# Kernel tuning notes

Hardware: AMD Instinct MI355X
Metric: run time of the kernel (lower is better)

Reference implementation:

```python
import jax, jax.numpy as jnp
import numpy as np

B, N, C, H = 4, 1024, 768, 12
HD = C // H
EPS = 1e-5


def setup_inputs() -> dict:
    key = jax.random.key(0)
    ks = jax.random.split(key, 6)
    before = jax.random.normal(ks[0], (B, N, C), dtype=jnp.float32)
    after = jax.random.normal(ks[1], (B, N, C), dtype=jnp.float32)
    W_qkv = jax.random.normal(ks[2], (3 * C, C), dtype=jnp.float32) * (1.0 / np.sqrt(C))
    ln_g = jnp.ones((HD,), dtype=jnp.float32)
    ln_b = jnp.zeros((HD,), dtype=jnp.float32)
    W_proj = jax.random.normal(ks[3], (C, C), dtype=jnp.float32) * (1.0 / np.sqrt(C))
    b_proj = jnp.zeros((C,), dtype=jnp.float32)
    return {"before": before, "after": after, "W_qkv": W_qkv, "ln_g": ln_g,
            "ln_b": ln_b, "W_proj": W_proj, "b_proj": b_proj}


def _qkv_norm(x, W_qkv, ln_g, ln_b):
    # x: [B,N,C] -> qkv: [3,B,H,N,hd] with LayerNorm over head_dim
    qkv = (x @ W_qkv.T).reshape(B, N, 3, H, HD).transpose(2, 0, 3, 1, 4)
    mu = jnp.mean(qkv, axis=-1, keepdims=True)
    var = jnp.var(qkv, axis=-1, keepdims=True)
    qkv = (qkv - mu) * jax.lax.rsqrt(var + EPS) * ln_g + ln_b
    return qkv[0], qkv[1], qkv[2]


def _cross_attn(q, k, v, scale, W_proj, b_proj):
    # q,k,v: [B,H,N,hd]
    attn = jax.nn.softmax(jnp.einsum('bhqd,bhkd->bhqk', q, k) * scale, axis=-1)
    ctx = jnp.einsum('bhqk,bhkd->bhqd', attn, v)  # [B,H,N,hd]
    ctx = ctx.transpose(0, 2, 1, 3).reshape(B, N, C)
    ctx = ctx @ W_proj.T + b_proj
    # NOTE: original adds q.reshape(B,N,C) WITHOUT transposing heads back; replicate faithfully.
    return ctx + q.reshape(B, N, C)


def reference(before, after, W_qkv, ln_g, ln_b, W_proj, b_proj):
    scale = HD ** (-0.5)
    q_b, k_b, v_b = _qkv_norm(before, W_qkv, ln_g, ln_b)
    q_a, k_a, v_a = _qkv_norm(after, W_qkv, ln_g, ln_b)
    context_a = _cross_attn(q_b, k_a, v_a, scale, W_proj, b_proj)
    context_b = _cross_attn(q_a, k_b, v_b, scale, W_proj, b_proj)
    return (context_b, context_a)
```

## Files before the change

### kernel.cpp

```cpp
#include <hip/hip_runtime.h>


typedef __bf16 bf16x8 __attribute__((ext_vector_type(8)));
typedef float  f32x4  __attribute__((ext_vector_type(4)));
typedef unsigned int u32x4 __attribute__((ext_vector_type(4)));
typedef unsigned short us;

#define MFMA16(a, b, c) __builtin_amdgcn_mfma_f32_16x16x32_bf16(a, b, c, 0, 0, 0)

#define C1F 0.18033688011112042f
#define INV_C1F 5.545177444479562f

__device__ __forceinline__ us f2bf(float f) {
  unsigned int u = __builtin_bit_cast(unsigned int, f);
  u += 0x7FFFu + ((u >> 16) & 1u);
  return (us)(u >> 16);
}
__device__ __forceinline__ float bf2f(us h) {
  unsigned int u = ((unsigned int)h) << 16;
  return __builtin_bit_cast(float, u);
}
__device__ __forceinline__ bf16x8 ld16(const us* p) {
  return __builtin_bit_cast(bf16x8, *(const u32x4*)p);
}
__device__ __forceinline__ unsigned int pkbf(float lo, float hi) {
  return __builtin_amdgcn_perm(__builtin_bit_cast(unsigned int, hi),
                               __builtin_bit_cast(unsigned int, lo),
                               0x07060302u);
}

#define CH 136

__global__ __launch_bounds__(256) void k_convert(
    const float* __restrict__ before, const float* __restrict__ after,
    const float* __restrict__ wqkv, const float* __restrict__ wproj,
    us* __restrict__ ws) {
  int t = blockIdx.x * 256 + threadIdx.x;
  us* dst; int u;
  if (t < 786432)       { u = t;           dst = ws; }
  else if (t < 1007616) { u = t - 786432;  dst = ws + 6291456; }
  else                  { u = t - 1007616; dst = ws + 8060928; }
  int l15 = u & 15, c2 = u >> 4;
  int kc = c2 % 96, mt = c2 / 96;
  int row = mt * 16 + l15;
  const float* srow;
  if (t < 786432)       srow = row < 4096 ? before + (size_t)row * 768
                                          : after + (size_t)(row - 4096) * 768;
  else if (t < 1007616) srow = wqkv + (size_t)row * 768;
  else                  srow = wproj + (size_t)row * 768;
  const float4* s4 = (const float4*)(srow + kc * 8);
  float4 a = s4[0], b = s4[1];
  union { u32x4 v; us s[8]; } o;
  o.s[0] = f2bf(a.x); o.s[1] = f2bf(a.y); o.s[2] = f2bf(a.z); o.s[3] = f2bf(a.w);
  o.s[4] = f2bf(b.x); o.s[5] = f2bf(b.y); o.s[6] = f2bf(b.z); o.s[7] = f2bf(b.w);
  *(u32x4*)(dst + (size_t)c2 * 128 + l15 * 8) = o.v;
}

template <int MT>
__device__ __forceinline__ void gemm_mainloop(
    const us* __restrict__ A, const us* __restrict__ B,
    int m0, int n0, us* As, us* Bs, f32x4 (&acc)[MT / 32][4]) {
  constexpr int AJ = MT / 32;
  constexpr int NITER = 12;
  const int tid = threadIdx.x, lane = tid & 63, w = tid >> 6;
  const int quad = lane >> 4, l15 = lane & 15;
  const int wm = (w >> 1) * (MT / 2), wn = (w & 1) * 64;
  u32x4 ra[2][AJ], rb[2][4];

  auto load_regs = [&](int s, int k0) {
#pragma unroll
    for (int j = 0; j < AJ; ++j) {
      int u = w * AJ + j;
      ra[s][j] = *(const u32x4*)(A + ((size_t)((m0 >> 4) + (u >> 1)) * 96
                                      + (k0 >> 3) + (u & 1) * 4) * 128 + lane * 8);
    }
#pragma unroll
    for (int j = 0; j < 4; ++j) {
      int u = w * 4 + j;
      rb[s][j] = *(const u32x4*)(B + ((size_t)((n0 >> 4) + (u >> 1)) * 96
                                      + (k0 >> 3) + (u & 1) * 4) * 128 + lane * 8);
    }
  };
  auto store_regs = [&](int s) {
#pragma unroll
    for (int j = 0; j < AJ; ++j) {
      int slot = (w * AJ + j) * 4 + quad;
      *(u32x4*)(As + slot * CH + l15 * 8) = ra[s][j];
    }
#pragma unroll
    for (int j = 0; j < 4; ++j) {
      int slot = (w * 4 + j) * 4 + quad;
      *(u32x4*)(Bs + slot * CH + l15 * 8) = rb[s][j];
    }
  };

  load_regs(0, 0);
  load_regs(1, 64);
  store_regs(0);
  __syncthreads();

#pragma unroll
  for (int it = 0; it < NITER; ++it) {
    if (it + 2 < NITER) load_regs(it & 1, (it + 2) * 64);
#pragma unroll
    for (int ks = 0; ks < 2; ++ks) {
      bf16x8 af[AJ], bfr[4];
#pragma unroll
      for (int mf = 0; mf < AJ; ++mf)
        af[mf] = ld16(As + (((wm >> 4) + mf) * 8 + ks * 4 + quad) * CH + l15 * 8);
#pragma unroll
      for (int nf = 0; nf < 4; ++nf)
        bfr[nf] = ld16(Bs + (((wn >> 4) + nf) * 8 + ks * 4 + quad) * CH + l15 * 8);
#pragma unroll
      for (int mf = 0; mf < AJ; ++mf)
#pragma unroll
        for (int nf = 0; nf < 4; ++nf)
          acc[mf][nf] = MFMA16(af[mf], bfr[nf], acc[mf][nf]);
    }
    __syncthreads();
    if (it + 1 < NITER) {
      store_regs((it + 1) & 1);
      __syncthreads();
    }
  }
}

__global__ __launch_bounds__(256) void k_gemm_qkv(
    const us* __restrict__ A, const us* __restrict__ B, us* __restrict__ Cqk,
    us* __restrict__ Vg, const float* __restrict__ g, const float* __restrict__ bb) {
  __shared__ us As[64 * CH];
  __shared__ us Bs[64 * CH];
  const int lane = threadIdx.x & 63, w = threadIdx.x >> 6;
  const int quad = lane >> 4, l15 = lane & 15;
  const int m0 = blockIdx.x * 128, n0 = blockIdx.y * 128;
  const int wm = (w >> 1) * 64, wn = (w & 1) * 64;
  f32x4 acc[4][4] = {};
  gemm_mainloop<128>(A, B, m0, n0, As, Bs, acc);

  float gl[4], bl[4];
#pragma unroll
  for (int nf = 0; nf < 4; ++nf) { gl[nf] = g[nf * 16 + l15]; bl[nf] = bb[nf * 16 + l15]; }

  if ((n0 + wn) < 1536) {
    const float qs = (n0 + wn) < 768 ? C1F : 1.0f;
#pragma unroll
    for (int mf = 0; mf < 4; ++mf)
#pragma unroll
      for (int r = 0; r < 4; ++r) {
        float s1 = acc[mf][0][r] + acc[mf][1][r] + acc[mf][2][r] + acc[mf][3][r];
        float s2 = acc[mf][0][r] * acc[mf][0][r] + acc[mf][1][r] * acc[mf][1][r]
                 + acc[mf][2][r] * acc[mf][2][r] + acc[mf][3][r] * acc[mf][3][r];
#pragma unroll
        for (int o = 1; o < 16; o <<= 1) { s1 += __shfl_xor(s1, o); s2 += __shfl_xor(s2, o); }
        float mu = s1 * (1.0f / 64.0f);
        float var = s2 * (1.0f / 64.0f) - mu * mu;
        float sc = rsqrtf(var + 1e-5f);
        size_t cb = ((size_t)(((m0 + wm) >> 4) + mf) * 192 + ((n0 + wn) >> 3)
                     + (l15 >> 3)) * 128 + (quad * 4 + r) * 8 + (l15 & 7);
#pragma unroll
        for (int nf = 0; nf < 4; ++nf)
          Cqk[cb + nf * 256] = f2bf(((acc[mf][nf][r] - mu) * sc * gl[nf] + bl[nf]) * qs);
      }
  } else {
    const int h = ((n0 + wn) - 1536) >> 6;
#pragma unroll
    for (int mf = 0; mf < 4; ++mf) {
      int mrow = m0 + wm + mf * 16;
      int s = mrow >> 12, b2 = (mrow >> 10) & 3;
      int K0 = mrow & 1023;
      int nfk = (K0 >> 4) & 3;
      us* vb = Vg + (size_t)(s * 48 + b2 * 12 + h) * 65536;
      float vv[4][4];
#pragma unroll
      for (int r = 0; r < 4; ++r) {
        float s1 = acc[mf][0][r] + acc[mf][1][r] + acc[mf][2][r] + acc[mf][3][r];
        float s2 = acc[mf][0][r] * acc[mf][0][r] + acc[mf][1][r] * acc[mf][1][r]
                 + acc[mf][2][r] * acc[mf][2][r] + acc[mf][3][r] * acc[mf][3][r];
#pragma unroll
        for (int o = 1; o < 16; o <<= 1) { s1 += __shfl_xor(s1, o); s2 += __shfl_xor(s2, o); }
        float mu = s1 * (1.0f / 64.0f);
        float var = s2 * (1.0f / 64.0f) - mu * mu;
        float sc = rsqrtf(var + 1e-5f);
#pragma unroll
        for (int nf = 0; nf < 4; ++nf)
          vv[nf][r] = (acc[mf][nf][r] - mu) * sc * gl[nf] + bl[nf];
      }
      size_t pchunk = ((size_t)(K0 >> 6) << 3) + ((nfk >> 1) << 2) + quad;
      int poff = l15 * 8 + (nfk & 1) * 4;
#pragma unroll
      for (int nf = 0; nf < 4; ++nf) {
        ushort4 o4;
        o4.x = f2bf(vv[nf][0]); o4.y = f2bf(vv[nf][1]);
        o4.z = f2bf(vv[nf][2]); o4.w = f2bf(vv[nf][3]);
        *(ushort4*)(vb + ((size_t)nf * 128 + pchunk) * 128 + poff) = o4;
      }
    }
  }
}

__global__ __launch_bounds__(256) void k_gemm_proj(
    const us* __restrict__ A, const us* __restrict__ B, float* __restrict__ C,
    const us* __restrict__ qkvr, const float* __restrict__ bias) {
  __shared__ us As[32 * CH];
  __shared__ us Bs[64 * CH];
  const int lane = threadIdx.x & 63, w = threadIdx.x >> 6;
  const int quad = lane >> 4, l15 = lane & 15;
  const int m0 = blockIdx.x * 64, n0 = blockIdx.y * 128;
  const int wm = (w >> 1) * 32, wn = (w & 1) * 64;
  f32x4 acc[2][4] = {};
  gemm_mainloop<64>(A, B, m0, n0, As, Bs, acc);

  const int cg = (n0 + wn) >> 6;
  float bl[4];
#pragma unroll
  for (int nf = 0; nf < 4; ++nf) bl[nf] = bias[n0 + wn + nf * 16 + l15];
#pragma unroll
  for (int mf = 0; mf < 2; ++mf)
#pragma unroll
    for (int r = 0; r < 4; ++r) {
      int row = m0 + wm + mf * 16 + quad * 4 + r;
      int hf = row >> 12;
      int m4 = row & 4095;
      int b = m4 >> 10, i = m4 & 1023;
      int j = i * 12 + cg;
      int h = j >> 10, n = j & 1023;
      int qrow = ((hf ^ 1) << 12) + (b << 10) + n;
      size_t rb2 = ((size_t)(qrow >> 4) * 192 + h * 8 + (l15 >> 3)) * 128
                 + (qrow & 15) * 8 + (l15 & 7);
      size_t base = (size_t)row * 768 + n0 + wn + l15;
#pragma unroll
      for (int nf = 0; nf < 4; ++nf)
        C[base + nf * 16] = acc[mf][nf][r] + bl[nf] + bf2f(qkvr[rb2 + nf * 256]) * INV_C1F;
    }
}

__global__ __launch_bounds__(256) void k_attn(const us* __restrict__ qkvr,
                                              const us* __restrict__ vtg,
                                              us* __restrict__ ctx) {
  __shared__ us Ks[2][32 * CH];
  __shared__ us Vt[2][32 * CH];
  const int tid = threadIdx.x, lane = tid & 63, w = tid >> 6;
  const int quad = lane >> 4, l15 = lane & 15;
  const int hi = blockIdx.x, qt = blockIdx.y;
  const int hf = hi / 48, bh = hi - hf * 48;
  const int b = bh / 12, h = bh - (bh / 12) * 12;
  const int ihq = hf ^ 1, ihk = hf;
  const int r0 = qt * 128 + w * 32;
  const int qmt = (ihq * 4096 + b * 1024 + r0) >> 4;
  const int kb16 = (ihk * 4096 + b * 1024) >> 4;
  const us* vbase = vtg + (size_t)(ihk * 48 + b * 12 + h) * 65536;

  bf16x8 aq[2][2];
#pragma unroll
  for (int mf = 0; mf < 2; ++mf)
#pragma unroll
    for (int ks = 0; ks < 2; ++ks)
      aq[mf][ks] = ld16(qkvr + ((size_t)(qmt + mf) * 192 + h * 8 + ks * 4 + quad) * 128
                        + l15 * 8);

  u32x4 rk[2][2], rv[2][2];
  auto load_kv = [&](int s, int kt) {
#pragma unroll
    for (int j = 0; j < 2; ++j) {
      int u = w * 2 + j;
      rk[s][j] = *(const u32x4*)(qkvr + ((size_t)(kb16 + kt * 4 + (u >> 1)) * 192
                                         + 96 + h * 8 + (u & 1) * 4) * 128 + lane * 8);
      rv[s][j] = *(const u32x4*)(vbase + ((size_t)(u >> 1) * 128 + kt * 8
                                          + (u & 1) * 4) * 128 + lane * 8);
    }
  };
  auto store_kv = [&](int s, int buf) {
#pragma unroll
    for (int j = 0; j < 2; ++j) {
      int slot = (w * 2 + j) * 4 + quad;
      *(u32x4*)(Ks[buf] + slot * CH + l15 * 8) = rk[s][j];
      *(u32x4*)(Vt[buf] + slot * CH + l15 * 8) = rv[s][j];
    }
  };

  f32x4 O[2][4] = {};
  float lsum[2] = {};

  auto step = [&](int kt, int p) {
    if (kt + 2 < 16) load_kv(p, kt + 2);

    f32x4 sT[2][4] = {};
#pragma unroll
    for (int ks = 0; ks < 2; ++ks)
#pragma unroll
      for (int nf = 0; nf < 4; ++nf) {
        bf16x8 kf = ld16(Ks[p] + (nf * 8 + ks * 4 + quad) * CH + l15 * 8);
        sT[0][nf] = MFMA16(kf, aq[0][ks], sT[0][nf]);
        sT[1][nf] = MFMA16(kf, aq[1][ks], sT[1][nf]);
      }

    bf16x8 pf[2][2];
#pragma unroll
    for (int mf = 0; mf < 2; ++mf) {
      float ev[4][4];
#pragma unroll
      for (int nf = 0; nf < 4; ++nf)
#pragma unroll
        for (int r = 0; r < 4; ++r)
          ev[nf][r] = __builtin_amdgcn_exp2f(sT[mf][nf][r]);
      lsum[mf] += ((ev[0][0] + ev[0][1]) + (ev[0][2] + ev[0][3]))
                + ((ev[1][0] + ev[1][1]) + (ev[1][2] + ev[1][3]))
                + ((ev[2][0] + ev[2][1]) + (ev[2][2] + ev[2][3]))
                + ((ev[3][0] + ev[3][1]) + (ev[3][2] + ev[3][3]));
#pragma unroll
      for (int k2 = 0; k2 < 2; ++k2) {
        u32x4 wds;
#pragma unroll
        for (int wd = 0; wd < 4; ++wd)
          wds[wd] = pkbf(ev[k2 * 2 + (wd >> 1)][(wd & 1) * 2],
                         ev[k2 * 2 + (wd >> 1)][(wd & 1) * 2 + 1]);
        pf[mf][k2] = __builtin_bit_cast(bf16x8, wds);
      }
    }

#pragma unroll
    for (int k2 = 0; k2 < 2; ++k2)
#pragma unroll
      for (int df = 0; df < 4; ++df) {
        bf16x8 av = ld16(Vt[p] + (df * 8 + k2 * 4 + quad) * CH + l15 * 8);
        O[0][df] = MFMA16(av, pf[0][k2], O[0][df]);
        O[1][df] = MFMA16(av, pf[1][k2], O[1][df]);
      }

    if (kt + 1 < 16) store_kv(p ^ 1, p ^ 1);
    __syncthreads();
  };

  load_kv(0, 0);
  load_kv(1, 1);
  store_kv(0, 0);
  __syncthreads();

  for (int kt = 0; kt < 16; kt += 2) {
    step(kt, 0);
    step(kt + 1, 1);
  }

  const int mc0 = hf * 256 + b * 64 + qt * 8 + w * 2;
#pragma unroll
  for (int mf = 0; mf < 2; ++mf) {
    float l = lsum[mf];
    l += __shfl_xor(l, 16);
    l += __shfl_xor(l, 32);
    float inv = 1.0f / l;
#pragma unroll
    for (int df = 0; df < 4; ++df) {
      ushort4 o4;
      o4.x = f2bf(O[mf][df][0] * inv); o4.y = f2bf(O[mf][df][1] * inv);
      o4.z = f2bf(O[mf][df][2] * inv); o4.w = f2bf(O[mf][df][3] * inv);
      *(ushort4*)(ctx + ((size_t)(mc0 + mf) * 96 + h * 8 + df * 2 + (quad >> 1)) * 128
                  + l15 * 8 + (quad & 1) * 4) = o4;
    }
  }
}

extern "C" void kernel_launch(void* const* d_in, const int* in_sizes, int n_in,
                              void* d_out, int out_size, void* d_ws, size_t ws_size,
                              hipStream_t stream) {
  (void)in_sizes; (void)n_in; (void)out_size; (void)ws_size;
  const float* before = (const float*)d_in[0];
  const float* after  = (const float*)d_in[1];
  const float* wqkv   = (const float*)d_in[2];
  const float* lng    = (const float*)d_in[3];
  const float* lnb    = (const float*)d_in[4];
  const float* wproj  = (const float*)d_in[5];
  const float* bproj  = (const float*)d_in[6];
  float* out = (float*)d_out;
  us* ws  = (us*)d_ws;
  us* xbt  = ws;
  us* wqt  = ws + 6291456;
  us* wpt  = ws + 8060928;
  us* qkvr = ws + 8650752;
  us* vtg  = ws + 21233664;
  us* ctx  = ws + 27525120;

  k_convert<<<4224, 256, 0, stream>>>(before, after, wqkv, wproj, ws);
  k_gemm_qkv<<<dim3(64, 18), 256, 0, stream>>>(xbt, wqt, qkvr, vtg, lng, lnb);
  k_attn<<<dim3(96, 8), 256, 0, stream>>>(qkvr, vtg, ctx);
  k_gemm_proj<<<dim3(128, 6), 256, 0, stream>>>(ctx, wpt, out, qkvr, bproj);
}
```

Before: 186.1 us.

## Load B fragments directly from global into registers and double-buffer A in LDS

The GEMM mainloop stops staging the B tile through shared memory. Each wave now loads its MFMA B fragments straight from the pre-packed global layout into registers, prefetched one K-step ahead. A is double-buffered in LDS, which drops one of the two barriers per iteration. This cuts LDS traffic and synchronisation, but costs more registers and more global loads, since the two wave rows of a block fetch the same B fragments separately.

After: 182.7 us. About the same (-1.8%).

```diff
diff --git a/kernel.cpp b/kernel.cpp
--- a/kernel.cpp
+++ b/kernel.cpp
@@ -59,83 +59,78 @@
 template <int MT>
 __device__ __forceinline__ void gemm_mainloop(
     const us* __restrict__ A, const us* __restrict__ B,
-    int m0, int n0, us* As, us* Bs, f32x4 (&acc)[MT / 32][4]) {
+    int m0, int n0, us* As, f32x4 (&acc)[MT / 32][4]) {
   constexpr int AJ = MT / 32;
+  constexpr int BUFC = (MT / 2) * CH;
   constexpr int NITER = 12;
   const int tid = threadIdx.x, lane = tid & 63, w = tid >> 6;
   const int quad = lane >> 4, l15 = lane & 15;
   const int wm = (w >> 1) * (MT / 2), wn = (w & 1) * 64;
-  u32x4 ra[2][AJ], rb[2][4];
-
-  auto load_regs = [&](int s, int k0) {
+  u32x4 ra[2][AJ];
+  u32x4 rbf[2][8];
+
+  auto load_a = [&](int s, int k0) {
 #pragma unroll
     for (int j = 0; j < AJ; ++j) {
       int u = w * AJ + j;
       ra[s][j] = *(const u32x4*)(A + ((size_t)((m0 >> 4) + (u >> 1)) * 96
                                       + (k0 >> 3) + (u & 1) * 4) * 128 + lane * 8);
     }
-#pragma unroll
-    for (int j = 0; j < 4; ++j) {
-      int u = w * 4 + j;
-      rb[s][j] = *(const u32x4*)(B + ((size_t)((n0 >> 4) + (u >> 1)) * 96
-                                      + (k0 >> 3) + (u & 1) * 4) * 128 + lane * 8);
-    }
-  };
-  auto store_regs = [&](int s) {
+  };
+  auto store_a = [&](int s, int buf) {
 #pragma unroll
     for (int j = 0; j < AJ; ++j) {
       int slot = (w * AJ + j) * 4 + quad;
-      *(u32x4*)(As + slot * CH + l15 * 8) = ra[s][j];
-    }
-#pragma unroll
-    for (int j = 0; j < 4; ++j) {
-      int slot = (w * 4 + j) * 4 + quad;
-      *(u32x4*)(Bs + slot * CH + l15 * 8) = rb[s][j];
-    }
-  };
-
-  load_regs(0, 0);
-  load_regs(1, 64);
-  store_regs(0);
+      *(u32x4*)(As + buf * BUFC + slot * CH + l15 * 8) = ra[s][j];
+    }
+  };
+  auto load_b = [&](int s, int k0) {
+#pragma unroll
+    for (int ks = 0; ks < 2; ++ks)
+#pragma unroll
+      for (int nf = 0; nf < 4; ++nf)
+        rbf[s][ks * 4 + nf] = *(const u32x4*)(B
+            + ((size_t)(((n0 + wn) >> 4) + nf) * 96 + (k0 >> 3) + ks * 4 + quad) * 128
+            + l15 * 8);
+  };
+
+  load_a(0, 0);
+  load_a(1, 64);
+  load_b(0, 0);
+  store_a(0, 0);
   __syncthreads();
 
 #pragma unroll
   for (int it = 0; it < NITER; ++it) {
-    if (it + 2 < NITER) load_regs(it & 1, (it + 2) * 64);
-#pragma unroll
-    for (int ks = 0; ks < 2; ++ks) {
-      bf16x8 af[AJ], bfr[4];
-#pragma unroll
-      for (int mf = 0; mf < AJ; ++mf)
-        af[mf] = ld16(As + (((wm >> 4) + mf) * 8 + ks * 4 + quad) * CH + l15 * 8);
-#pragma unroll
-      for (int nf = 0; nf < 4; ++nf)
-        bfr[nf] = ld16(Bs + (((wn >> 4) + nf) * 8 + ks * 4 + quad) * CH + l15 * 8);
-#pragma unroll
-      for (int mf = 0; mf < AJ; ++mf)
+    const int p = it & 1;
+    if (it + 2 < NITER) load_a(p, (it + 2) * 64);
+    if (it + 1 < NITER) load_b(p ^ 1, (it + 1) * 64);
+#pragma unroll
+    for (int ks = 0; ks < 2; ++ks)
+#pragma unroll
+      for (int mf = 0; mf < AJ; ++mf) {
+        bf16x8 af = ld16(As + p * BUFC + (((wm >> 4) + mf) * 8 + ks * 4 + quad) * CH
+                         + l15 * 8);
 #pragma unroll
         for (int nf = 0; nf < 4; ++nf)
-          acc[mf][nf] = MFMA16(af[mf], bfr[nf], acc[mf][nf]);
-    }
+          acc[mf][nf] = MFMA16(af, __builtin_bit_cast(bf16x8, rbf[p][ks * 4 + nf]),
+                               acc[mf][nf]);
+      }
+    if (it + 1 < NITER) store_a(p ^ 1, p ^ 1);
     __syncthreads();
-    if (it + 1 < NITER) {
-      store_regs((it + 1) & 1);
-      __syncthreads();
-    }
   }
 }
 
 __global__ __launch_bounds__(256) void k_gemm_qkv(
     const us* __restrict__ A, const us* __restrict__ B, us* __restrict__ Cqk,
     us* __restrict__ Vg, const float* __restrict__ g, const float* __restrict__ bb) {
-  __shared__ us As[64 * CH];
-  __shared__ us Bs[64 * CH];
+  __shared__ us As[128 * CH];
   const int lane = threadIdx.x & 63, w = threadIdx.x >> 6;
   const int quad = lane >> 4, l15 = lane & 15;
   const int m0 = blockIdx.x * 128, n0 = blockIdx.y * 128;
   const int wm = (w >> 1) * 64, wn = (w & 1) * 64;
   f32x4 acc[4][4] = {};
-  gemm_mainloop<128>(A, B, m0, n0, As, Bs, acc);
+  gemm_mainloop<128>(A, B, m0, n0, As, acc);
 
   float gl[4], bl[4];
 #pragma unroll
@@ -201,14 +196,13 @@
 __global__ __launch_bounds__(256) void k_gemm_proj(
     const us* __restrict__ A, const us* __restrict__ B, float* __restrict__ C,
     const us* __restrict__ qkvr, const float* __restrict__ bias) {
-  __shared__ us As[32 * CH];
-  __shared__ us Bs[64 * CH];
+  __shared__ us As[64 * CH];
   const int lane = threadIdx.x & 63, w = threadIdx.x >> 6;
   const int quad = lane >> 4, l15 = lane & 15;
   const int m0 = blockIdx.x * 64, n0 = blockIdx.y * 128;
   const int wm = (w >> 1) * 32, wn = (w & 1) * 64;
   f32x4 acc[2][4] = {};
-  gemm_mainloop<64>(A, B, m0, n0, As, Bs, acc);
+  gemm_mainloop<64>(A, B, m0, n0, As, acc);
 
   const int cg = (n0 + wn) >> 6;
   float bl[4];
```
